# Kernel tuning notes

Measured on AMD Instinct MI355X. Metric: run time of the kernel, lower is better.

The kernel has to match this reference:

```python
import jax, jax.numpy as jnp
import numpy as np

D_MODEL = 1024
D_HEAD = 64  # d_model / num_heads
NEG_INF = -1e9  # matches torch code's -1000000000.0 additive mask


def setup_inputs() -> dict:
    key = jax.random.key(0)
    ks = jax.random.split(key, 9)
    B, S = 4, 4096
    scale = 0.02
    return {
        "q": jax.random.normal(ks[0], (B, S, D_MODEL), dtype=jnp.float32),
        "k": jax.random.normal(ks[1], (B, S, D_MODEL), dtype=jnp.float32),
        "v": jax.random.normal(ks[2], (B, S, D_MODEL), dtype=jnp.float32),
        "WQ_w": jax.random.normal(ks[3], (D_HEAD, D_MODEL), dtype=jnp.float32) * scale,
        "WQ_b": jax.random.normal(ks[4], (D_HEAD,), dtype=jnp.float32) * scale,
        "WK_w": jax.random.normal(ks[5], (D_HEAD, D_MODEL), dtype=jnp.float32) * scale,
        "WK_b": jax.random.normal(ks[6], (D_HEAD,), dtype=jnp.float32) * scale,
        "WV_w": jax.random.normal(ks[7], (D_HEAD, D_MODEL), dtype=jnp.float32) * scale,
        "WV_b": jax.random.normal(ks[8], (D_HEAD,), dtype=jnp.float32) * scale,
    }


def reference(q, k, v, WQ_w, WQ_b, WK_w, WK_b, WV_w, WV_b):
    # Linear projections (torch nn.Linear: x @ W.T + b)
    qh = jnp.einsum("bsd,hd->bsh", q, WQ_w) + WQ_b  # [B,S,64]
    kh = jnp.einsum("bsd,hd->bsh", k, WK_w) + WK_b
    vh = jnp.einsum("bsd,hd->bsh", v, WV_w) + WV_b
    # Scaled dot-product scores [B,S,S]
    scores = jnp.einsum("bqh,bkh->bqk", qh, kh) / np.sqrt(D_HEAD).astype(np.float32)
    # Causal additive mask: upper triangle (j > i) gets -1e9
    S = scores.shape[-1]
    causal = jnp.triu(jnp.ones((S, S), dtype=scores.dtype), k=1) * NEG_INF
    scores = scores + causal
    attn = jax.nn.softmax(scores, axis=-1)
    out = jnp.einsum("bqk,bkh->bqh", attn, vh)  # [B,S,64]
    # Dropout is identity in eval mode (deterministic reference)
    return out
```

## Files before the change

### kernel.cpp

```cpp
#include <hip/hip_runtime.h>

#define SEQ 4096
#define DM  1024
#define DH  64
#define NB  4

typedef __attribute__((ext_vector_type(4))) float  f32x4;
typedef __attribute__((ext_vector_type(8))) __bf16 bf16x8;

__device__ __forceinline__ unsigned short f2bf(float f) {
    unsigned int u = __float_as_uint(f);
    u += 0x7FFFu + ((u >> 16) & 1u);
    return (unsigned short)(u >> 16);
}

__device__ __forceinline__ f32x4 mfma_bf16(bf16x8 a, bf16x8 b, f32x4 c) {
    return __builtin_amdgcn_mfma_f32_16x16x32_bf16(a, b, c, 0, 0, 0);
}

__global__ __launch_bounds__(256) void proj_kernel(
    const float* __restrict__ xq, const float* __restrict__ xk, const float* __restrict__ xv,
    const float* __restrict__ Wq, const float* __restrict__ bq,
    const float* __restrict__ Wk, const float* __restrict__ bk,
    const float* __restrict__ Wv, const float* __restrict__ bv,
    unsigned short* __restrict__ qh, unsigned short* __restrict__ kh,
    unsigned short* __restrict__ vhT)
{
    __shared__ unsigned short x_tile[64][72];
    __shared__ unsigned short w_tile[64][72];

    const int which = blockIdx.y;
    const float* X  = (which == 0) ? xq : (which == 1) ? xk : xv;
    const float* W  = (which == 0) ? Wq : (which == 1) ? Wk : Wv;
    const float* Bb = (which == 0) ? bq : (which == 1) ? bk : bv;

    const int m0   = blockIdx.x * 64;
    const int t    = threadIdx.x;
    const int wv   = t >> 6;
    const int lane = t & 63;
    const int quad = lane >> 4;
    const int l16  = lane & 15;
    const int sr   = t >> 2;
    const int sc   = (t & 3) << 4;

    f32x4 acc[4];
#pragma unroll
    for (int i = 0; i < 4; ++i) acc[i] = f32x4{0.f, 0.f, 0.f, 0.f};

    for (int kc = 0; kc < DM; kc += 64) {
        __syncthreads();
        const float* xg = X + (size_t)(m0 + sr) * DM + (kc + sc);
        const float* wg = W + (size_t)sr * DM + (kc + sc);
#pragma unroll
        for (int i = 0; i < 4; ++i) {
            f32x4 xvv = *(const f32x4*)(xg + i * 4);
            f32x4 wvv = *(const f32x4*)(wg + i * 4);
            ushort4 xs = make_ushort4(f2bf(xvv[0]), f2bf(xvv[1]), f2bf(xvv[2]), f2bf(xvv[3]));
            ushort4 ws = make_ushort4(f2bf(wvv[0]), f2bf(wvv[1]), f2bf(wvv[2]), f2bf(wvv[3]));
            *(ushort4*)&x_tile[sr][sc + i * 4] = xs;
            *(ushort4*)&w_tile[sr][sc + i * 4] = ws;
        }
        __syncthreads();
#pragma unroll
        for (int ks = 0; ks < 2; ++ks) {
            bf16x8 a = *(const bf16x8*)&x_tile[wv * 16 + l16][ks * 32 + quad * 8];
#pragma unroll
            for (int nt = 0; nt < 4; ++nt) {
                bf16x8 b = *(const bf16x8*)&w_tile[nt * 16 + l16][ks * 32 + quad * 8];
                acc[nt] = mfma_bf16(a, b, acc[nt]);
            }
        }
    }

    __syncthreads();
#pragma unroll
    for (int nt = 0; nt < 4; ++nt) {
        float bias = Bb[nt * 16 + l16];
#pragma unroll
        for (int r = 0; r < 4; ++r)
            x_tile[wv * 16 + quad * 4 + r][nt * 16 + l16] = f2bf(acc[nt][r] + bias);
    }
    __syncthreads();

    if (which < 2) {
        unsigned short* out = (which == 0) ? qh : kh;
        unsigned short* og  = out + (size_t)(m0 + sr) * DH + sc;
        *(int4*)og       = *(const int4*)&x_tile[sr][sc];
        *(int4*)(og + 8) = *(const int4*)&x_tile[sr][sc + 8];
    } else {
        const int bb = m0 >> 12;
        const int s0 = m0 & 4095;
        const int h  = sr;
        const int r0 = sc;
        __align__(16) unsigned short tmp[16];
#pragma unroll
        for (int i = 0; i < 16; ++i) tmp[i] = x_tile[r0 + i][h];
        unsigned short* og = vhT + (size_t)bb * DH * SEQ + (size_t)h * SEQ + (s0 + r0);
        *(int4*)og       = *(const int4*)&tmp[0];
        *(int4*)(og + 8) = *(const int4*)&tmp[8];
    }
}

__global__ __launch_bounds__(256) void attn_kernel(
    const unsigned short* __restrict__ qh, const unsigned short* __restrict__ kh,
    const unsigned short* __restrict__ vhT, float* __restrict__ out)
{
    __shared__ unsigned short k_t[64][72];
    __shared__ unsigned short v_t[64][72];
    __shared__ unsigned short qp[64][72];

    const int qt   = blockIdx.x;
    const int b    = blockIdx.y;
    const int t    = threadIdx.x;
    const int wv   = t >> 6;
    const int lane = t & 63;
    const int quad = lane >> 4;
    const int l16  = lane & 15;
    const int sr   = t >> 2;
    const int sc   = (t & 3) << 4;

    const size_t base = (size_t)b * SEQ * DH;

    {
        const unsigned short* g = qh + base + (size_t)(qt * 64 + sr) * DH + sc;
        *(int4*)&qp[sr][sc]     = *(const int4*)g;
        *(int4*)&qp[sr][sc + 8] = *(const int4*)(g + 8);
    }
    __syncthreads();
    bf16x8 qfrag[2];
    qfrag[0] = *(const bf16x8*)&qp[wv * 16 + l16][quad * 8];
    qfrag[1] = *(const bf16x8*)&qp[wv * 16 + l16][32 + quad * 8];

    f32x4 o_acc[4];
#pragma unroll
    for (int i = 0; i < 4; ++i) o_acc[i] = f32x4{0.f, 0.f, 0.f, 0.f};
    float m_i[4], l_i[4];
#pragma unroll
    for (int r = 0; r < 4; ++r) { m_i[r] = -1e30f; l_i[r] = 0.f; }

    const int rowb = wv * 16 + quad * 4;

    for (int jt = 0; jt <= qt; ++jt) {
        __syncthreads();
        {
            const unsigned short* kg = kh + base + (size_t)(jt * 64 + sr) * DH + sc;
            *(int4*)&k_t[sr][sc]     = *(const int4*)kg;
            *(int4*)&k_t[sr][sc + 8] = *(const int4*)(kg + 8);
            const unsigned short* vg = vhT + (size_t)b * DH * SEQ + (size_t)sr * SEQ + (jt * 64 + sc);
            *(int4*)&v_t[sr][sc]     = *(const int4*)vg;
            *(int4*)&v_t[sr][sc + 8] = *(const int4*)(vg + 8);
        }
        __syncthreads();

        f32x4 s_acc[4];
#pragma unroll
        for (int i = 0; i < 4; ++i) s_acc[i] = f32x4{0.f, 0.f, 0.f, 0.f};
#pragma unroll
        for (int ks = 0; ks < 2; ++ks) {
#pragma unroll
            for (int nt = 0; nt < 4; ++nt) {
                bf16x8 bfr = *(const bf16x8*)&k_t[nt * 16 + l16][ks * 32 + quad * 8];
                s_acc[nt] = mfma_bf16(qfrag[ks], bfr, s_acc[nt]);
            }
        }

        const bool diag = (jt == qt);
#pragma unroll
        for (int nt = 0; nt < 4; ++nt) {
            const int col = nt * 16 + l16;
#pragma unroll
            for (int r = 0; r < 4; ++r) {
                float sv = s_acc[nt][r] * 0.125f;
                if (diag && (col > rowb + r)) sv = -1e30f;
                s_acc[nt][r] = sv;
            }
        }

        float mx[4];
#pragma unroll
        for (int r = 0; r < 4; ++r)
            mx[r] = fmaxf(fmaxf(s_acc[0][r], s_acc[1][r]), fmaxf(s_acc[2][r], s_acc[3][r]));
#pragma unroll
        for (int off = 1; off < 16; off <<= 1)
#pragma unroll
            for (int r = 0; r < 4; ++r)
                mx[r] = fmaxf(mx[r], __shfl_xor(mx[r], off, 64));

        float alpha[4];
#pragma unroll
        for (int r = 0; r < 4; ++r) {
            float mn = fmaxf(m_i[r], mx[r]);
            alpha[r] = __expf(m_i[r] - mn);
            m_i[r]   = mn;
        }

        float rs[4] = {0.f, 0.f, 0.f, 0.f};
#pragma unroll
        for (int nt = 0; nt < 4; ++nt)
#pragma unroll
            for (int r = 0; r < 4; ++r) {
                float p = __expf(s_acc[nt][r] - m_i[r]);
                s_acc[nt][r] = p;
                rs[r] += p;
            }
#pragma unroll
        for (int off = 1; off < 16; off <<= 1)
#pragma unroll
            for (int r = 0; r < 4; ++r)
                rs[r] += __shfl_xor(rs[r], off, 64);
#pragma unroll
        for (int r = 0; r < 4; ++r) l_i[r] = l_i[r] * alpha[r] + rs[r];

#pragma unroll
        for (int nt = 0; nt < 4; ++nt)
#pragma unroll
            for (int r = 0; r < 4; ++r)
                qp[rowb + r][nt * 16 + l16] = f2bf(s_acc[nt][r]);

#pragma unroll
        for (int nt = 0; nt < 4; ++nt)
#pragma unroll
            for (int r = 0; r < 4; ++r)
                o_acc[nt][r] *= alpha[r];

#pragma unroll
        for (int ks = 0; ks < 2; ++ks) {
            bf16x8 pa = *(const bf16x8*)&qp[wv * 16 + l16][ks * 32 + quad * 8];
#pragma unroll
            for (int nt = 0; nt < 4; ++nt) {
                bf16x8 vb = *(const bf16x8*)&v_t[nt * 16 + l16][ks * 32 + quad * 8];
                o_acc[nt] = mfma_bf16(pa, vb, o_acc[nt]);
            }
        }
    }

    float inv[4];
#pragma unroll
    for (int r = 0; r < 4; ++r) inv[r] = 1.0f / l_i[r];
#pragma unroll
    for (int nt = 0; nt < 4; ++nt)
#pragma unroll
        for (int r = 0; r < 4; ++r)
            out[base + (size_t)(qt * 64 + rowb + r) * DH + nt * 16 + l16] = o_acc[nt][r] * inv[r];
}

extern "C" void kernel_launch(void* const* d_in, const int* in_sizes, int n_in,
                              void* d_out, int out_size, void* d_ws, size_t ws_size,
                              hipStream_t stream)
{
    (void)in_sizes; (void)n_in; (void)out_size; (void)ws_size;
    const float* q  = (const float*)d_in[0];
    const float* k  = (const float*)d_in[1];
    const float* v  = (const float*)d_in[2];
    const float* Wq = (const float*)d_in[3];
    const float* bq = (const float*)d_in[4];
    const float* Wk = (const float*)d_in[5];
    const float* bk = (const float*)d_in[6];
    const float* Wv = (const float*)d_in[7];
    const float* bv = (const float*)d_in[8];
    float* out = (float*)d_out;

    unsigned short* qh  = (unsigned short*)d_ws;
    unsigned short* kh  = qh + (size_t)NB * SEQ * DH;
    unsigned short* vhT = kh + (size_t)NB * SEQ * DH;

    proj_kernel<<<dim3(NB * SEQ / 64, 3), 256, 0, stream>>>(
        q, k, v, Wq, bq, Wk, bk, Wv, bv, qh, kh, vhT);
    attn_kernel<<<dim3(SEQ / 64, NB), 256, 0, stream>>>(qh, kh, vhT, out);
}
```

Measured before the change: 326.2 us.

## Split causal attention across KV chunks with a merge pass; prefetch projection loads

The attention kernel is split flash-decoding style. Each query tile's causal KV range is cut into chunks of 8 tiles, each handled by its own block, which writes unnormalized partial outputs plus row max and sum to workspace. A separate merge kernel rescales and combines the partials. This is meant to fix load imbalance and low occupancy from the triangular workload of only 256 blocks, at the cost of extra partial-result memory traffic and a third launch. The projection kernel also register-prefetches the next K-chunk of global loads while the current chunk runs its MFMAs.

```diff
diff --git a/kernel.cpp b/kernel.cpp
--- a/kernel.cpp
+++ b/kernel.cpp
@@ -4,6 +4,7 @@
 #define DM  1024
 #define DH  64
 #define NB  4
+#define SLOTS_PER_B 288
 
 typedef __attribute__((ext_vector_type(4))) float  f32x4;
 typedef __attribute__((ext_vector_type(8))) __bf16 bf16x8;
@@ -47,20 +48,29 @@
 #pragma unroll
     for (int i = 0; i < 4; ++i) acc[i] = f32x4{0.f, 0.f, 0.f, 0.f};
 
+    const float* xg = X + (size_t)(m0 + sr) * DM + sc;
+    const float* wg = W + (size_t)sr * DM + sc;
+
+    f32x4 xr[4], wr[4];
+#pragma unroll
+    for (int i = 0; i < 4; ++i) { xr[i] = *(const f32x4*)(xg + i * 4); wr[i] = *(const f32x4*)(wg + i * 4); }
+
     for (int kc = 0; kc < DM; kc += 64) {
         __syncthreads();
-        const float* xg = X + (size_t)(m0 + sr) * DM + (kc + sc);
-        const float* wg = W + (size_t)sr * DM + (kc + sc);
 #pragma unroll
         for (int i = 0; i < 4; ++i) {
-            f32x4 xvv = *(const f32x4*)(xg + i * 4);
-            f32x4 wvv = *(const f32x4*)(wg + i * 4);
-            ushort4 xs = make_ushort4(f2bf(xvv[0]), f2bf(xvv[1]), f2bf(xvv[2]), f2bf(xvv[3]));
-            ushort4 ws = make_ushort4(f2bf(wvv[0]), f2bf(wvv[1]), f2bf(wvv[2]), f2bf(wvv[3]));
-            *(ushort4*)&x_tile[sr][sc + i * 4] = xs;
-            *(ushort4*)&w_tile[sr][sc + i * 4] = ws;
+            *(ushort4*)&x_tile[sr][sc + i * 4] =
+                make_ushort4(f2bf(xr[i][0]), f2bf(xr[i][1]), f2bf(xr[i][2]), f2bf(xr[i][3]));
+            *(ushort4*)&w_tile[sr][sc + i * 4] =
+                make_ushort4(f2bf(wr[i][0]), f2bf(wr[i][1]), f2bf(wr[i][2]), f2bf(wr[i][3]));
         }
         __syncthreads();
+        if (kc + 64 < DM) {
+            const float* xn = xg + kc + 64;
+            const float* wn = wg + kc + 64;
+#pragma unroll
+            for (int i = 0; i < 4; ++i) { xr[i] = *(const f32x4*)(xn + i * 4); wr[i] = *(const f32x4*)(wn + i * 4); }
+        }
 #pragma unroll
         for (int ks = 0; ks < 2; ++ks) {
             bf16x8 a = *(const bf16x8*)&x_tile[wv * 16 + l16][ks * 32 + quad * 8];
@@ -101,16 +111,26 @@
     }
 }
 
-__global__ __launch_bounds__(256) void attn_kernel(
+__global__ __launch_bounds__(256) void attn_split_kernel(
     const unsigned short* __restrict__ qh, const unsigned short* __restrict__ kh,
-    const unsigned short* __restrict__ vhT, float* __restrict__ out)
+    const unsigned short* __restrict__ vhT,
+    float* __restrict__ pO, float* __restrict__ pm, float* __restrict__ pl)
 {
+    const int chunk = blockIdx.x;
+    const int qt    = blockIdx.y;
+    const int b     = blockIdx.z;
+    const int nc    = (qt + 8) >> 3;
+    if (chunk >= nc) return;
+
+    const int g = qt >> 3, rr = qt & 7;
+    const int slot = b * SLOTS_PER_B + 4 * g * (g + 1) + rr * (g + 1) + chunk;
+    const int c0 = chunk * 8;
+    const int c1 = min(c0 + 8, qt + 1);
+
     __shared__ unsigned short k_t[64][72];
     __shared__ unsigned short v_t[64][72];
     __shared__ unsigned short qp[64][72];
 
-    const int qt   = blockIdx.x;
-    const int b    = blockIdx.y;
     const int t    = threadIdx.x;
     const int wv   = t >> 6;
     const int lane = t & 63;
@@ -122,9 +142,9 @@
     const size_t base = (size_t)b * SEQ * DH;
 
     {
-        const unsigned short* g = qh + base + (size_t)(qt * 64 + sr) * DH + sc;
-        *(int4*)&qp[sr][sc]     = *(const int4*)g;
-        *(int4*)&qp[sr][sc + 8] = *(const int4*)(g + 8);
+        const unsigned short* gq = qh + base + (size_t)(qt * 64 + sr) * DH + sc;
+        *(int4*)&qp[sr][sc]     = *(const int4*)gq;
+        *(int4*)&qp[sr][sc + 8] = *(const int4*)(gq + 8);
     }
     __syncthreads();
     bf16x8 qfrag[2];
@@ -140,7 +160,7 @@
 
     const int rowb = wv * 16 + quad * 4;
 
-    for (int jt = 0; jt <= qt; ++jt) {
+    for (int jt = c0; jt < c1; ++jt) {
         __syncthreads();
         {
             const unsigned short* kg = kh + base + (size_t)(jt * 64 + sr) * DH + sc;
@@ -234,14 +254,60 @@
         }
     }
 
-    float inv[4];
-#pragma unroll
-    for (int r = 0; r < 4; ++r) inv[r] = 1.0f / l_i[r];
+    float* po = pO + (size_t)slot * 4096;
 #pragma unroll
     for (int nt = 0; nt < 4; ++nt)
 #pragma unroll
         for (int r = 0; r < 4; ++r)
-            out[base + (size_t)(qt * 64 + rowb + r) * DH + nt * 16 + l16] = o_acc[nt][r] * inv[r];
+            po[(rowb + r) * 64 + nt * 16 + l16] = o_acc[nt][r];
+    if (l16 == 0) {
+#pragma unroll
+        for (int r = 0; r < 4; ++r) {
+            pm[slot * 64 + rowb + r] = m_i[r];
+            pl[slot * 64 + rowb + r] = l_i[r];
+        }
+    }
+}
+
+__global__ __launch_bounds__(256) void attn_merge_kernel(
+    const float* __restrict__ pO, const float* __restrict__ pm, const float* __restrict__ pl,
+    float* __restrict__ out)
+{
+    const int qt = blockIdx.x;
+    const int b  = blockIdx.y;
+    const int nc = (qt + 8) >> 3;
+    const int g = qt >> 3, rr = qt & 7;
+    const int s0 = b * SLOTS_PER_B + 4 * g * (g + 1) + rr * (g + 1);
+
+    const int t   = threadIdx.x;
+    const int row = t >> 2;
+    const int c0  = (t & 3) << 4;
+
+    float mstar = -1e30f;
+    for (int c = 0; c < nc; ++c)
+        mstar = fmaxf(mstar, pm[(s0 + c) * 64 + row]);
+
+    f32x4 acc[4];
+#pragma unroll
+    for (int i = 0; i < 4; ++i) acc[i] = f32x4{0.f, 0.f, 0.f, 0.f};
+    float lsum = 0.f;
+
+    for (int c = 0; c < nc; ++c) {
+        const float w = __expf(pm[(s0 + c) * 64 + row] - mstar);
+        lsum += w * pl[(s0 + c) * 64 + row];
+        const float* p = pO + (size_t)(s0 + c) * 4096 + row * 64 + c0;
+#pragma unroll
+        for (int i = 0; i < 4; ++i) {
+            f32x4 v = *(const f32x4*)(p + i * 4);
+            acc[i] += w * v;
+        }
+    }
+
+    const float inv = 1.0f / lsum;
+    float* og = out + (size_t)b * SEQ * DH + (size_t)(qt * 64 + row) * DH + c0;
+#pragma unroll
+    for (int i = 0; i < 4; ++i)
+        *(f32x4*)(og + i * 4) = acc[i] * inv;
 }
 
 extern "C" void kernel_launch(void* const* d_in, const int* in_sizes, int n_in,
@@ -263,8 +329,12 @@
     unsigned short* qh  = (unsigned short*)d_ws;
     unsigned short* kh  = qh + (size_t)NB * SEQ * DH;
     unsigned short* vhT = kh + (size_t)NB * SEQ * DH;
+    float* pO = (float*)(vhT + (size_t)NB * SEQ * DH);
+    float* pm = pO + (size_t)NB * SLOTS_PER_B * 4096;
+    float* pl = pm + (size_t)NB * SLOTS_PER_B * 64;
 
     proj_kernel<<<dim3(NB * SEQ / 64, 3), 256, 0, stream>>>(
         q, k, v, Wq, bq, Wk, bk, Wv, bv, qh, kh, vhT);
-    attn_kernel<<<dim3(SEQ / 64, NB), 256, 0, stream>>>(qh, kh, vhT, out);
-}
+    attn_split_kernel<<<dim3(8, SEQ / 64, NB), 256, 0, stream>>>(qh, kh, vhT, pO, pm, pl);
+    attn_merge_kernel<<<dim3(SEQ / 64, NB), 256, 0, stream>>>(pO, pm, pl, out);
+}
```

Result: faster. 281.3 us (-13.8%).
